# Performance work log

Measured on AMD Instinct MI355X. Metric: run time of the kernel, lower is better.

The kernel has to match this reference:

```python
import jax, jax.numpy as jnp
import numpy as np

B = 32768        # batch
COORD = 64       # entorhinal coordinate dim
DG = 2048        # dentate gyrus dim
CA3 = 256        # CA3 dim
CA1 = 256        # CA1 dim
K_ACTIVE = max(1, int(DG * 0.04))   # = 81, DG top-k sparsity
SETTLE_STEPS = 5
GAIN = 0.7
SIGMA = 2.0      # ca3_distance_sigma
N_EPISODES = 64  # ca3_max_episodes
EC_TAU = 0.5
LN_EPS = 1e-5
COS_EPS = 1e-8


def _build_w_recurrent():
    """Hebbian outer-product weights gated by anatomical distance mask (numpy, deterministic)."""
    rng = np.random.default_rng(0)
    theta = np.linspace(0.0, np.pi, CA3)
    pos = np.stack([3.0 * np.cos(theta),
                    4.0 + np.sin(theta),
                    rng.standard_normal(CA3) * 0.8], axis=-1)
    pos = pos + rng.standard_normal(pos.shape) * 0.15
    diff = pos[None, :, :] - pos[:, None, :]
    dist = np.sqrt((diff ** 2).sum(-1) + 1e-8)
    mask = np.exp(-dist / SIGMA)                       # [CA3, CA3] distance gate
    P = rng.standard_normal((N_EPISODES, CA3)).astype(np.float32)
    P = P / (np.linalg.norm(P, axis=1, keepdims=True) + 1e-8)
    W = P.T @ P                                        # Hebbian pattern storage
    np.fill_diagonal(W, 0.0)
    W = W * mask
    return jnp.asarray(W, dtype=jnp.float32)


def setup_inputs() -> dict:
    key = jax.random.key(0)
    ks = jax.random.split(key, 16)
    def lin(k, out_d, in_d):
        s = 1.0 / np.sqrt(in_d)
        return jax.random.uniform(k, (out_d, in_d), jnp.float32, -s, s)
    return {
        "coords":   jax.random.normal(ks[0], (B, COORD), jnp.float32),
        # EC layernorm
        "ec_gamma": jnp.ones((COORD,), jnp.float32),
        "ec_beta":  jnp.zeros((COORD,), jnp.float32),
        # DG perforant path + layernorm
        "W_pp":     lin(ks[1], DG, COORD),
        "b_pp":     jnp.zeros((DG,), jnp.float32),
        "dg_gamma": jnp.ones((DG,), jnp.float32),
        "dg_beta":  jnp.zeros((DG,), jnp.float32),
        # CA3
        "W_mossy":  lin(ks[2], CA3, DG),
        "W_rec":    _build_w_recurrent(),
        "W_sc":     lin(ks[3], CA1, CA3),
        "b_sc":     jnp.zeros((CA1,), jnp.float32),
        # CA1 comparator
        "W_ta":     lin(ks[4], CA1, COORD),
        "b_ta":     jnp.zeros((CA1,), jnp.float32),
        "W_cs":     lin(ks[5], CA1, CA1),
        "W_cd":     lin(ks[6], CA1, CA1),
        "W_og":     lin(ks[7], CA1, CA1),
        "b_og":     jnp.zeros((CA1,), jnp.float32),
    }


def _layernorm(x, gamma, beta):
    mu = jnp.mean(x, axis=-1, keepdims=True)
    var = jnp.mean(jnp.square(x - mu), axis=-1, keepdims=True)
    return (x - mu) * jax.lax.rsqrt(var + LN_EPS) * gamma + beta


def reference(coords, ec_gamma, ec_beta, W_pp, b_pp, dg_gamma, dg_beta,
              W_mossy, W_rec, W_sc, b_sc, W_ta, b_ta, W_cs, W_cd, W_og, b_og):
    # --- EntorhinalCortex: short-term buffer (no-grad EMA from zero init) + layernorm ---
    buf = EC_TAU * 0.0 + (1.0 - EC_TAU) * jax.lax.stop_gradient(jnp.mean(coords, axis=0))
    ec = _layernorm(coords + 0.1 * buf[None, :], ec_gamma, ec_beta)          # [B, COORD]

    # --- DentateGyrus: relu -> layernorm -> top-k sparsification (scatter) ---
    proj = _layernorm(jax.nn.relu(ec @ W_pp.T + b_pp), dg_gamma, dg_beta)    # [B, DG]
    vals, idx = jax.lax.top_k(proj, K_ACTIVE)                                # [B, K]
    rows = jnp.arange(proj.shape[0])[:, None]
    dg = jnp.zeros_like(proj).at[rows, idx].set(vals)                        # sparse code

    # --- CA3AttractorNetwork: mossy cue + recurrent attractor settle ---
    cue = dg @ W_mossy.T                                                     # [B, CA3]
    state = cue
    for _ in range(SETTLE_STEPS):
        state = jnp.tanh(GAIN * (state @ W_rec.T) + (1.0 - GAIN) * cue)
    ca1_input = state @ W_sc.T + b_sc                                        # [B, CA1]

    # --- CA1Comparator: novelty-gated mix of direct EC path and schaffer input ---
    direct = ec @ W_ta.T + b_ta                                              # [B, CA1]
    s_proj = ca1_input @ W_cs.T
    d_proj = direct @ W_cd.T
    s_n = jnp.maximum(jnp.linalg.norm(s_proj, axis=-1), COS_EPS)
    d_n = jnp.maximum(jnp.linalg.norm(d_proj, axis=-1), COS_EPS)
    cos_sim = jnp.sum(s_proj * d_proj, axis=-1) / (s_n * d_n)
    novelty = jnp.clip(1.0 - cos_sim, 0.0, 1.0)                              # [B]
    gate = novelty[:, None]
    combined = gate * direct + (1.0 - gate) * ca1_input
    ca1_output = jnp.tanh(combined @ W_og.T + b_og)                          # [B, CA1]
    return ca1_output, novelty
```

## Files before the change

### kernel.cpp

```cpp
#include <hip/hip_runtime.h>
#include <hip/hip_bf16.h>
#include <math.h>

#define B_N 32768
#define COORD 64
#define DG 2048
#define CA 256
#define K_ACT 81
#define SETTLE_STEPS 5
#define GAIN 0.7f
#define LN_EPS 1e-5f
#define COS_EPS 1e-8f

__device__ __forceinline__ float wave_sum(float v) {
#pragma unroll
  for (int d = 1; d < 64; d <<= 1) v += __shfl_xor(v, d);
  return v;
}

__device__ __forceinline__ float dot4(float4 a, float4 b) {
  return a.x * b.x + a.y * b.y + a.z * b.z + a.w * b.w;
}

__device__ __forceinline__ void fma4(float4& a, float s, float4 w) {
  a.x += s * w.x; a.y += s * w.y; a.z += s * w.z; a.w += s * w.w;
}

__device__ __forceinline__ unsigned int okey(float f) {
  unsigned int u = __float_as_uint(f);
  return (u & 0x80000000u) ? ~u : (u | 0x80000000u);
}

__global__ void colsum_kernel(const float* __restrict__ coords,
                              float* __restrict__ colsum) {
  int tid = threadIdx.x;
  int col = tid & 63;
  int rg = tid >> 6;
  float s = 0.f;
  int base = blockIdx.x * 128;
#pragma unroll 4
  for (int i = 0; i < 32; ++i) {
    int r = base + rg + i * 4;
    s += coords[r * COORD + col];
  }
  __shared__ float sh[256];
  sh[tid] = s;
  __syncthreads();
  if (tid < 64) {
    float t = sh[tid] + sh[tid + 64] + sh[tid + 128] + sh[tid + 192];
    atomicAdd(&colsum[tid], t);
  }
}

__global__ void transpose_any(const float* __restrict__ S,
                              float* __restrict__ T, int R, int C) {
  int idx = blockIdx.x * 256 + threadIdx.x;
  if (idx < R * C) {
    int r = idx / C, c = idx - r * C;
    T[c * R + r] = S[r * C + c];
  }
}

__global__ __launch_bounds__(512, 4) void mega1(
    const float* __restrict__ coords, const float* __restrict__ colsum,
    const float* __restrict__ ec_gamma, const float* __restrict__ ec_beta,
    const float* __restrict__ W_ppT, const float* __restrict__ b_pp,
    const float* __restrict__ dg_gamma, const float* __restrict__ dg_beta,
    const float* __restrict__ WmT, float* __restrict__ cue_g) {
  __shared__ __align__(16) float proj_s[8][DG];
  __shared__ __align__(16) float ec_s[8][COORD];
  __shared__ unsigned int hist[8][256];
  __shared__ float psum_s[8][8], psq_s[8][8];
  __shared__ int sel_s[8][88];

  const int w = threadIdx.x >> 6;
  const int l = threadIdx.x & 63;
  const int row0 = blockIdx.x * 8;

  {
    int row = row0 + w;
    float x = coords[row * COORD + l] + (0.05f / (float)B_N) * colsum[l];
    float mu = wave_sum(x) * (1.f / 64.f);
    float d = x - mu;
    float var = wave_sum(d * d) * (1.f / 64.f);
    ec_s[w][l] = d * rsqrtf(var + LN_EPS) * ec_gamma[l] + ec_beta[l];
  }
  __syncthreads();

  {
    float4 acc[8];
#pragma unroll
    for (int r = 0; r < 8; ++r) acc[r] = make_float4(0.f, 0.f, 0.f, 0.f);
    const float4* wp4 = reinterpret_cast<const float4*>(W_ppT);
    const int cbase = 64 * w + l;
    for (int kg = 0; kg < 16; ++kg) {
      float4 w40 = wp4[(4 * kg + 0) * 512 + cbase];
      float4 w41 = wp4[(4 * kg + 1) * 512 + cbase];
      float4 w42 = wp4[(4 * kg + 2) * 512 + cbase];
      float4 w43 = wp4[(4 * kg + 3) * 512 + cbase];
#pragma unroll
      for (int r = 0; r < 8; ++r) {
        float4 e4 = reinterpret_cast<const float4*>(ec_s[r])[kg];
        fma4(acc[r], e4.x, w40);
        fma4(acc[r], e4.y, w41);
        fma4(acc[r], e4.z, w42);
        fma4(acc[r], e4.w, w43);
      }
    }
    float4 bp = reinterpret_cast<const float4*>(b_pp)[cbase];
#pragma unroll
    for (int r = 0; r < 8; ++r) {
      float4 h;
      h.x = fmaxf(acc[r].x + bp.x, 0.f);
      h.y = fmaxf(acc[r].y + bp.y, 0.f);
      h.z = fmaxf(acc[r].z + bp.z, 0.f);
      h.w = fmaxf(acc[r].w + bp.w, 0.f);
      reinterpret_cast<float4*>(proj_s[r])[cbase] = h;
      float ps = wave_sum(h.x + h.y + h.z + h.w);
      float pq = wave_sum(dot4(h, h));
      if (l == 0) { psum_s[w][r] = ps; psq_s[w][r] = pq; }
    }
  }
  __syncthreads();

  float mu2, rs2;
  {
    float s = 0.f, q = 0.f;
#pragma unroll
    for (int w2 = 0; w2 < 8; ++w2) { s += psum_s[w2][w]; q += psq_s[w2][w]; }
    mu2 = s * (1.f / (float)DG);
    float var = q * (1.f / (float)DG) - mu2 * mu2;
    rs2 = rsqrtf(var + LN_EPS);
  }
  unsigned int key[32];
#pragma unroll 4
  for (int i = 0; i < 32; ++i) {
    int j = i * 64 + l;
    float v = (proj_s[w][j] - mu2) * rs2 * dg_gamma[j] + dg_beta[j];
    proj_s[w][j] = v;
    key[i] = okey(v);
  }

  unsigned int prefix = 0, rem = K_ACT;
#pragma unroll 1
  for (int pass = 0; pass < 4; ++pass) {
    int sh = 24 - 8 * pass;
#pragma unroll
    for (int b = l; b < 256; b += 64) hist[w][b] = 0;
#pragma unroll 4
    for (int i = 0; i < 32; ++i) {
      unsigned int k = key[i];
      bool ok = (pass == 0) || ((k >> (sh + 8)) == prefix);
      if (ok) atomicAdd(&hist[w][(k >> sh) & 255u], 1u);
    }
    unsigned int h0 = hist[w][4 * l + 0], h1 = hist[w][4 * l + 1];
    unsigned int h2 = hist[w][4 * l + 2], h3 = hist[w][4 * l + 3];
    unsigned int own = h0 + h1 + h2 + h3;
    unsigned int inc = own;
#pragma unroll
    for (int d = 1; d < 64; d <<= 1) {
      unsigned int v = __shfl_down(inc, d);
      if (l + d < 64) inc += v;
    }
    unsigned int cnt = inc - own;
    unsigned int pk = 0;
    {
      unsigned int hb;
      hb = h3; if (cnt < rem && rem <= cnt + hb) pk = ((rem - cnt) << 8) | (unsigned)(4 * l + 3); cnt += hb;
      hb = h2; if (cnt < rem && rem <= cnt + hb) pk = ((rem - cnt) << 8) | (unsigned)(4 * l + 2); cnt += hb;
      hb = h1; if (cnt < rem && rem <= cnt + hb) pk = ((rem - cnt) << 8) | (unsigned)(4 * l + 1); cnt += hb;
      hb = h0; if (cnt < rem && rem <= cnt + hb) pk = ((rem - cnt) << 8) | (unsigned)(4 * l + 0); cnt += hb;
    }
#pragma unroll
    for (int d = 1; d < 64; d <<= 1) pk |= __shfl_xor(pk, d);
    prefix = (prefix << 8) | (pk & 255u);
    rem = pk >> 8;
  }
  const unsigned int Tkey = prefix;
  const unsigned int rem_final = rem;

  const unsigned long long below = (1ull << l) - 1ull;
  int basec = 0;
  unsigned int eq_seen = 0;
  for (int i = 0; i < 32; ++i) {
    int j = i * 64 + l;
    unsigned int k = key[i];
    bool gt = k > Tkey;
    bool eq = (k == Tkey);
    unsigned long long em = __ballot(eq);
    unsigned int eq_before = eq_seen + (unsigned)__popcll(em & below);
    bool sel = gt || (eq && (eq_before < rem_final));
    unsigned long long sm = __ballot(sel);
    int pos = basec + (int)__popcll(sm & below);
    if (sel) sel_s[w][pos] = j;
    basec += (int)__popcll(sm);
    eq_seen += (unsigned)__popcll(em);
  }

  float4 c4 = make_float4(0.f, 0.f, 0.f, 0.f);
  const float4* wm4 = reinterpret_cast<const float4*>(WmT);
  for (int k = 0; k < K_ACT; ++k) {
    int j = sel_s[w][k];
    float v = proj_s[w][j];
    fma4(c4, v, wm4[j * 64 + l]);
  }
  reinterpret_cast<float4*>(cue_g)[(size_t)(row0 + w) * 64 + l] = c4;
}

__global__ __launch_bounds__(256, 2) void mega2(
    const float* __restrict__ coords, const float* __restrict__ colsum,
    const float* __restrict__ ec_gamma, const float* __restrict__ ec_beta,
    const float* __restrict__ cue_g,
    const float* __restrict__ W_recT,
    const float* __restrict__ W_scT, const float* __restrict__ b_sc,
    const float* __restrict__ W_taT, const float* __restrict__ b_ta,
    const float* __restrict__ W_csT, const float* __restrict__ W_cdT,
    const float* __restrict__ W_ogT, const float* __restrict__ b_og,
    float* __restrict__ out) {
  __shared__ __align__(16) float bufA[32][CA];
  __shared__ __align__(16) float bufB[32][CA];
  __shared__ __align__(16) float ec_s[32][COORD];

  const int w = threadIdx.x >> 6;
  const int l = threadIdx.x & 63;
  const int row0 = blockIdx.x * 32 + w * 8;

#pragma unroll 1
  for (int r = 0; r < 8; ++r) {
    int row = row0 + r;
    float x = coords[row * COORD + l] + (0.05f / (float)B_N) * colsum[l];
    float mu = wave_sum(x) * (1.f / 64.f);
    float d = x - mu;
    float var = wave_sum(d * d) * (1.f / 64.f);
    ec_s[w * 8 + r][l] = d * rsqrtf(var + LN_EPS) * ec_gamma[l] + ec_beta[l];
  }

  float4 cu[8];
#pragma unroll
  for (int r = 0; r < 8; ++r) {
    cu[r] = reinterpret_cast<const float4*>(cue_g)[(size_t)(row0 + r) * 64 + l];
    reinterpret_cast<float4*>(bufA[w * 8 + r])[l] = cu[r];
  }

  const float4* wr4 = reinterpret_cast<const float4*>(W_recT);
  float4 acc[8];

#pragma unroll 1
  for (int it = 0; it < SETTLE_STEPS; ++it) {
#pragma unroll
    for (int r = 0; r < 8; ++r) acc[r] = make_float4(0.f, 0.f, 0.f, 0.f);
#pragma unroll 2
    for (int jg = 0; jg < 64; ++jg) {
      float4 w40 = wr4[(4 * jg + 0) * 64 + l];
      float4 w41 = wr4[(4 * jg + 1) * 64 + l];
      float4 w42 = wr4[(4 * jg + 2) * 64 + l];
      float4 w43 = wr4[(4 * jg + 3) * 64 + l];
#pragma unroll
      for (int r = 0; r < 8; ++r) {
        float4 s4 = reinterpret_cast<const float4*>(bufA[w * 8 + r])[jg];
        fma4(acc[r], s4.x, w40);
        fma4(acc[r], s4.y, w41);
        fma4(acc[r], s4.z, w42);
        fma4(acc[r], s4.w, w43);
      }
    }
#pragma unroll
    for (int r = 0; r < 8; ++r) {
      float4 ns;
      ns.x = tanhf(GAIN * acc[r].x + (1.f - GAIN) * cu[r].x);
      ns.y = tanhf(GAIN * acc[r].y + (1.f - GAIN) * cu[r].y);
      ns.z = tanhf(GAIN * acc[r].z + (1.f - GAIN) * cu[r].z);
      ns.w = tanhf(GAIN * acc[r].w + (1.f - GAIN) * cu[r].w);
      reinterpret_cast<float4*>(bufA[w * 8 + r])[l] = ns;
    }
  }

  {
    const float4* ws4 = reinterpret_cast<const float4*>(W_scT);
#pragma unroll
    for (int r = 0; r < 8; ++r) acc[r] = make_float4(0.f, 0.f, 0.f, 0.f);
#pragma unroll 2
    for (int jg = 0; jg < 64; ++jg) {
      float4 w40 = ws4[(4 * jg + 0) * 64 + l];
      float4 w41 = ws4[(4 * jg + 1) * 64 + l];
      float4 w42 = ws4[(4 * jg + 2) * 64 + l];
      float4 w43 = ws4[(4 * jg + 3) * 64 + l];
#pragma unroll
      for (int r = 0; r < 8; ++r) {
        float4 s4 = reinterpret_cast<const float4*>(bufA[w * 8 + r])[jg];
        fma4(acc[r], s4.x, w40);
        fma4(acc[r], s4.y, w41);
        fma4(acc[r], s4.z, w42);
        fma4(acc[r], s4.w, w43);
      }
    }
    float4 bs = reinterpret_cast<const float4*>(b_sc)[l];
#pragma unroll
    for (int r = 0; r < 8; ++r) {
      cu[r].x = acc[r].x + bs.x;
      cu[r].y = acc[r].y + bs.y;
      cu[r].z = acc[r].z + bs.z;
      cu[r].w = acc[r].w + bs.w;
      reinterpret_cast<float4*>(bufB[w * 8 + r])[l] = cu[r];
    }
  }

  float4 dr[8];
  {
    const float4* wt4 = reinterpret_cast<const float4*>(W_taT);
#pragma unroll
    for (int r = 0; r < 8; ++r) acc[r] = make_float4(0.f, 0.f, 0.f, 0.f);
#pragma unroll 2
    for (int kg = 0; kg < 16; ++kg) {
      float4 w40 = wt4[(4 * kg + 0) * 64 + l];
      float4 w41 = wt4[(4 * kg + 1) * 64 + l];
      float4 w42 = wt4[(4 * kg + 2) * 64 + l];
      float4 w43 = wt4[(4 * kg + 3) * 64 + l];
#pragma unroll
      for (int r = 0; r < 8; ++r) {
        float4 e4 = reinterpret_cast<const float4*>(ec_s[w * 8 + r])[kg];
        fma4(acc[r], e4.x, w40);
        fma4(acc[r], e4.y, w41);
        fma4(acc[r], e4.z, w42);
        fma4(acc[r], e4.w, w43);
      }
    }
    float4 bt = reinterpret_cast<const float4*>(b_ta)[l];
#pragma unroll
    for (int r = 0; r < 8; ++r) {
      dr[r].x = acc[r].x + bt.x;
      dr[r].y = acc[r].y + bt.y;
      dr[r].z = acc[r].z + bt.z;
      dr[r].w = acc[r].w + bt.w;
      reinterpret_cast<float4*>(bufA[w * 8 + r])[l] = dr[r];
    }
  }

  float4 dpr[8];
  {
    const float4* wc4 = reinterpret_cast<const float4*>(W_cdT);
#pragma unroll
    for (int r = 0; r < 8; ++r) acc[r] = make_float4(0.f, 0.f, 0.f, 0.f);
#pragma unroll 2
    for (int jg = 0; jg < 64; ++jg) {
      float4 w40 = wc4[(4 * jg + 0) * 64 + l];
      float4 w41 = wc4[(4 * jg + 1) * 64 + l];
      float4 w42 = wc4[(4 * jg + 2) * 64 + l];
      float4 w43 = wc4[(4 * jg + 3) * 64 + l];
#pragma unroll
      for (int r = 0; r < 8; ++r) {
        float4 s4 = reinterpret_cast<const float4*>(bufA[w * 8 + r])[jg];
        fma4(acc[r], s4.x, w40);
        fma4(acc[r], s4.y, w41);
        fma4(acc[r], s4.z, w42);
        fma4(acc[r], s4.w, w43);
      }
    }
#pragma unroll
    for (int r = 0; r < 8; ++r) dpr[r] = acc[r];
  }

  {
    const float4* wc4 = reinterpret_cast<const float4*>(W_csT);
#pragma unroll
    for (int r = 0; r < 8; ++r) acc[r] = make_float4(0.f, 0.f, 0.f, 0.f);
#pragma unroll 2
    for (int jg = 0; jg < 64; ++jg) {
      float4 w40 = wc4[(4 * jg + 0) * 64 + l];
      float4 w41 = wc4[(4 * jg + 1) * 64 + l];
      float4 w42 = wc4[(4 * jg + 2) * 64 + l];
      float4 w43 = wc4[(4 * jg + 3) * 64 + l];
#pragma unroll
      for (int r = 0; r < 8; ++r) {
        float4 s4 = reinterpret_cast<const float4*>(bufB[w * 8 + r])[jg];
        fma4(acc[r], s4.x, w40);
        fma4(acc[r], s4.y, w41);
        fma4(acc[r], s4.z, w42);
        fma4(acc[r], s4.w, w43);
      }
    }
  }

#pragma unroll 1
  for (int r = 0; r < 8; ++r) {
    float sd = wave_sum(dot4(acc[r], dpr[r]));
    float sn = wave_sum(dot4(acc[r], acc[r]));
    float dn = wave_sum(dot4(dpr[r], dpr[r]));
    float s_n = fmaxf(sqrtf(sn), COS_EPS);
    float d_n = fmaxf(sqrtf(dn), COS_EPS);
    float nov = fminf(fmaxf(1.f - sd / (s_n * d_n), 0.f), 1.f);
    float4 cb;
    cb.x = nov * dr[r].x + (1.f - nov) * cu[r].x;
    cb.y = nov * dr[r].y + (1.f - nov) * cu[r].y;
    cb.z = nov * dr[r].z + (1.f - nov) * cu[r].z;
    cb.w = nov * dr[r].w + (1.f - nov) * cu[r].w;
    reinterpret_cast<float4*>(bufA[w * 8 + r])[l] = cb;
    if (l == 0) out[(size_t)B_N * CA + (row0 + r)] = nov;
  }

  {
    const float4* wo4 = reinterpret_cast<const float4*>(W_ogT);
#pragma unroll
    for (int r = 0; r < 8; ++r) acc[r] = make_float4(0.f, 0.f, 0.f, 0.f);
#pragma unroll 2
    for (int jg = 0; jg < 64; ++jg) {
      float4 w40 = wo4[(4 * jg + 0) * 64 + l];
      float4 w41 = wo4[(4 * jg + 1) * 64 + l];
      float4 w42 = wo4[(4 * jg + 2) * 64 + l];
      float4 w43 = wo4[(4 * jg + 3) * 64 + l];
#pragma unroll
      for (int r = 0; r < 8; ++r) {
        float4 s4 = reinterpret_cast<const float4*>(bufA[w * 8 + r])[jg];
        fma4(acc[r], s4.x, w40);
        fma4(acc[r], s4.y, w41);
        fma4(acc[r], s4.z, w42);
        fma4(acc[r], s4.w, w43);
      }
    }
    float4 bo = reinterpret_cast<const float4*>(b_og)[l];
#pragma unroll
    for (int r = 0; r < 8; ++r) {
      float4 o;
      o.x = tanhf(acc[r].x + bo.x);
      o.y = tanhf(acc[r].y + bo.y);
      o.z = tanhf(acc[r].z + bo.z);
      o.w = tanhf(acc[r].w + bo.w);
      reinterpret_cast<float4*>(out)[(size_t)(row0 + r) * 64 + l] = o;
    }
  }
}

extern "C" void kernel_launch(void* const* d_in, const int* in_sizes, int n_in,
                              void* d_out, int out_size, void* d_ws,
                              size_t ws_size, hipStream_t stream) {
  const float* coords = (const float*)d_in[0];
  const float* ec_gamma = (const float*)d_in[1];
  const float* ec_beta = (const float*)d_in[2];
  const float* W_pp = (const float*)d_in[3];
  const float* b_pp = (const float*)d_in[4];
  const float* dg_gamma = (const float*)d_in[5];
  const float* dg_beta = (const float*)d_in[6];
  const float* W_mossy = (const float*)d_in[7];
  const float* W_rec = (const float*)d_in[8];
  const float* W_sc = (const float*)d_in[9];
  const float* b_sc = (const float*)d_in[10];
  const float* W_ta = (const float*)d_in[11];
  const float* b_ta = (const float*)d_in[12];
  const float* W_cs = (const float*)d_in[13];
  const float* W_cd = (const float*)d_in[14];
  const float* W_og = (const float*)d_in[15];
  const float* b_og = (const float*)d_in[16];
  float* out = (float*)d_out;

  float* ws = (float*)d_ws;
  float* colsum = ws;
  float* WmT = colsum + 64;
  float* W_ppT = WmT + 2048 * 256;
  float* W_recT = W_ppT + 64 * 2048;
  float* W_scT = W_recT + 256 * 256;
  float* W_csT = W_scT + 256 * 256;
  float* W_cdT = W_csT + 256 * 256;
  float* W_ogT = W_cdT + 256 * 256;
  float* W_taT = W_ogT + 256 * 256;
  float* cue_g = W_taT + 64 * 256;

  hipMemsetAsync(colsum, 0, COORD * sizeof(float), stream);
  colsum_kernel<<<256, 256, 0, stream>>>(coords, colsum);
  transpose_any<<<(256 * 2048 + 255) / 256, 256, 0, stream>>>(W_mossy, WmT, 256, 2048);
  transpose_any<<<(2048 * 64 + 255) / 256, 256, 0, stream>>>(W_pp, W_ppT, 2048, 64);
  transpose_any<<<(256 * 256 + 255) / 256, 256, 0, stream>>>(W_rec, W_recT, 256, 256);
  transpose_any<<<(256 * 256 + 255) / 256, 256, 0, stream>>>(W_sc, W_scT, 256, 256);
  transpose_any<<<(256 * 256 + 255) / 256, 256, 0, stream>>>(W_cs, W_csT, 256, 256);
  transpose_any<<<(256 * 256 + 255) / 256, 256, 0, stream>>>(W_cd, W_cdT, 256, 256);
  transpose_any<<<(256 * 256 + 255) / 256, 256, 0, stream>>>(W_og, W_ogT, 256, 256);
  transpose_any<<<(256 * 64 + 255) / 256, 256, 0, stream>>>(W_ta, W_taT, 256, 64);

  mega1<<<B_N / 8, 512, 0, stream>>>(coords, colsum, ec_gamma, ec_beta, W_ppT,
                                     b_pp, dg_gamma, dg_beta, WmT, cue_g);
  mega2<<<B_N / 32, 256, 0, stream>>>(coords, colsum, ec_gamma, ec_beta, cue_g,
                                      W_recT, W_scT, b_sc, W_taT, b_ta, W_csT,
                                      W_cdT, W_ogT, b_og, out);
}
```

Measured before the change: 1.059 ms.

## Pre-multiply chained linear weights and replace tanhf with exp-based tanh

Folds the linear chains W_cs·W_sc, W_cd·W_ta, W_og·W_sc and W_og·W_ta into combined weight matrices and bias vectors in small per-call setup kernels. The novelty-gated combine then becomes a linear mix of two precomputed projections, which removes one 256x256 matmul per row and the second shared buffer. tanhf is replaced by an __expf-based formula, and launch bounds are raised to allow more resident blocks. In exchange, floating-point reassociation shifts rounding, and the exp-based tanh can lose accuracy near zero.

```diff
diff --git a/kernel.cpp b/kernel.cpp
--- a/kernel.cpp
+++ b/kernel.cpp
@@ -24,6 +24,11 @@
 
 __device__ __forceinline__ void fma4(float4& a, float s, float4 w) {
   a.x += s * w.x; a.y += s * w.y; a.z += s * w.z; a.w += s * w.w;
+}
+
+__device__ __forceinline__ float fast_tanh(float x) {
+  float e = __expf(2.0f * x);
+  return 1.0f - 2.0f / (e + 1.0f);
 }
 
 __device__ __forceinline__ unsigned int okey(float f) {
@@ -58,6 +63,26 @@
   if (idx < R * C) {
     int r = idx / C, c = idx - r * C;
     T[c * R + r] = S[r * C + c];
+  }
+}
+
+__global__ void fuse_mm(const float* __restrict__ A, const float* __restrict__ BT,
+                        const float* __restrict__ bvec, float* __restrict__ FT,
+                        float* __restrict__ cvec) {
+  __shared__ float brow[256];
+  int in = blockIdx.x, out = threadIdx.x;
+  brow[out] = BT[in * 256 + out];
+  __syncthreads();
+  const float* arow = A + out * 256;
+  float acc = 0.f;
+#pragma unroll 4
+  for (int k = 0; k < 256; ++k) acc += arow[k] * brow[k];
+  FT[in * 256 + out] = acc;
+  if (in == 0) {
+    float b = 0.f;
+#pragma unroll 4
+    for (int k = 0; k < 256; ++k) b += arow[k] * bvec[k];
+    cvec[out] = b;
   }
 }
 
@@ -207,18 +232,16 @@
   reinterpret_cast<float4*>(cue_g)[(size_t)(row0 + w) * 64 + l] = c4;
 }
 
-__global__ __launch_bounds__(256, 2) void mega2(
+__global__ __launch_bounds__(256, 4) void mega2(
     const float* __restrict__ coords, const float* __restrict__ colsum,
     const float* __restrict__ ec_gamma, const float* __restrict__ ec_beta,
-    const float* __restrict__ cue_g,
-    const float* __restrict__ W_recT,
-    const float* __restrict__ W_scT, const float* __restrict__ b_sc,
-    const float* __restrict__ W_taT, const float* __restrict__ b_ta,
-    const float* __restrict__ W_csT, const float* __restrict__ W_cdT,
-    const float* __restrict__ W_ogT, const float* __restrict__ b_og,
-    float* __restrict__ out) {
-  __shared__ __align__(16) float bufA[32][CA];
-  __shared__ __align__(16) float bufB[32][CA];
+    const float* __restrict__ cue_g, const float* __restrict__ W_recT,
+    const float* __restrict__ F1T, const float* __restrict__ c1,
+    const float* __restrict__ F2T, const float* __restrict__ c2,
+    const float* __restrict__ F3T, const float* __restrict__ c3,
+    const float* __restrict__ F4T, const float* __restrict__ c4v,
+    const float* __restrict__ b_og, float* __restrict__ out) {
+  __shared__ __align__(16) float st_s[32][CA];
   __shared__ __align__(16) float ec_s[32][COORD];
 
   const int w = threadIdx.x >> 6;
@@ -239,148 +262,98 @@
 #pragma unroll
   for (int r = 0; r < 8; ++r) {
     cu[r] = reinterpret_cast<const float4*>(cue_g)[(size_t)(row0 + r) * 64 + l];
-    reinterpret_cast<float4*>(bufA[w * 8 + r])[l] = cu[r];
-  }
-
-  const float4* wr4 = reinterpret_cast<const float4*>(W_recT);
+    reinterpret_cast<float4*>(st_s[w * 8 + r])[l] = cu[r];
+  }
+
   float4 acc[8];
 
+  {
+    const float4* wr4 = reinterpret_cast<const float4*>(W_recT);
 #pragma unroll 1
-  for (int it = 0; it < SETTLE_STEPS; ++it) {
+    for (int it = 0; it < SETTLE_STEPS; ++it) {
+#pragma unroll
+      for (int r = 0; r < 8; ++r) acc[r] = make_float4(0.f, 0.f, 0.f, 0.f);
+#pragma unroll 2
+      for (int jg = 0; jg < 64; ++jg) {
+        float4 w40 = wr4[(4 * jg + 0) * 64 + l];
+        float4 w41 = wr4[(4 * jg + 1) * 64 + l];
+        float4 w42 = wr4[(4 * jg + 2) * 64 + l];
+        float4 w43 = wr4[(4 * jg + 3) * 64 + l];
+#pragma unroll
+        for (int r = 0; r < 8; ++r) {
+          float4 s4 = reinterpret_cast<const float4*>(st_s[w * 8 + r])[jg];
+          fma4(acc[r], s4.x, w40);
+          fma4(acc[r], s4.y, w41);
+          fma4(acc[r], s4.z, w42);
+          fma4(acc[r], s4.w, w43);
+        }
+      }
+#pragma unroll
+      for (int r = 0; r < 8; ++r) {
+        float4 ns;
+        ns.x = fast_tanh(GAIN * acc[r].x + (1.f - GAIN) * cu[r].x);
+        ns.y = fast_tanh(GAIN * acc[r].y + (1.f - GAIN) * cu[r].y);
+        ns.z = fast_tanh(GAIN * acc[r].z + (1.f - GAIN) * cu[r].z);
+        ns.w = fast_tanh(GAIN * acc[r].w + (1.f - GAIN) * cu[r].w);
+        reinterpret_cast<float4*>(st_s[w * 8 + r])[l] = ns;
+      }
+    }
+  }
+
+  float4 dpr[8];
+  {
+    const float4* f4 = reinterpret_cast<const float4*>(F2T);
+#pragma unroll
+    for (int r = 0; r < 8; ++r) dpr[r] = make_float4(0.f, 0.f, 0.f, 0.f);
+#pragma unroll 2
+    for (int kg = 0; kg < 16; ++kg) {
+      float4 w40 = f4[(4 * kg + 0) * 64 + l];
+      float4 w41 = f4[(4 * kg + 1) * 64 + l];
+      float4 w42 = f4[(4 * kg + 2) * 64 + l];
+      float4 w43 = f4[(4 * kg + 3) * 64 + l];
+#pragma unroll
+      for (int r = 0; r < 8; ++r) {
+        float4 e4 = reinterpret_cast<const float4*>(ec_s[w * 8 + r])[kg];
+        fma4(dpr[r], e4.x, w40);
+        fma4(dpr[r], e4.y, w41);
+        fma4(dpr[r], e4.z, w42);
+        fma4(dpr[r], e4.w, w43);
+      }
+    }
+    float4 cb = reinterpret_cast<const float4*>(c2)[l];
+#pragma unroll
+    for (int r = 0; r < 8; ++r) {
+      dpr[r].x += cb.x; dpr[r].y += cb.y; dpr[r].z += cb.z; dpr[r].w += cb.w;
+    }
+  }
+
+  {
+    const float4* f4 = reinterpret_cast<const float4*>(F1T);
 #pragma unroll
     for (int r = 0; r < 8; ++r) acc[r] = make_float4(0.f, 0.f, 0.f, 0.f);
 #pragma unroll 2
     for (int jg = 0; jg < 64; ++jg) {
-      float4 w40 = wr4[(4 * jg + 0) * 64 + l];
-      float4 w41 = wr4[(4 * jg + 1) * 64 + l];
-      float4 w42 = wr4[(4 * jg + 2) * 64 + l];
-      float4 w43 = wr4[(4 * jg + 3) * 64 + l];
-#pragma unroll
-      for (int r = 0; r < 8; ++r) {
-        float4 s4 = reinterpret_cast<const float4*>(bufA[w * 8 + r])[jg];
+      float4 w40 = f4[(4 * jg + 0) * 64 + l];
+      float4 w41 = f4[(4 * jg + 1) * 64 + l];
+      float4 w42 = f4[(4 * jg + 2) * 64 + l];
+      float4 w43 = f4[(4 * jg + 3) * 64 + l];
+#pragma unroll
+      for (int r = 0; r < 8; ++r) {
+        float4 s4 = reinterpret_cast<const float4*>(st_s[w * 8 + r])[jg];
         fma4(acc[r], s4.x, w40);
         fma4(acc[r], s4.y, w41);
         fma4(acc[r], s4.z, w42);
         fma4(acc[r], s4.w, w43);
       }
     }
+    float4 cb = reinterpret_cast<const float4*>(c1)[l];
 #pragma unroll
     for (int r = 0; r < 8; ++r) {
-      float4 ns;
-      ns.x = tanhf(GAIN * acc[r].x + (1.f - GAIN) * cu[r].x);
-      ns.y = tanhf(GAIN * acc[r].y + (1.f - GAIN) * cu[r].y);
-      ns.z = tanhf(GAIN * acc[r].z + (1.f - GAIN) * cu[r].z);
-      ns.w = tanhf(GAIN * acc[r].w + (1.f - GAIN) * cu[r].w);
-      reinterpret_cast<float4*>(bufA[w * 8 + r])[l] = ns;
-    }
-  }
-
-  {
-    const float4* ws4 = reinterpret_cast<const float4*>(W_scT);
-#pragma unroll
-    for (int r = 0; r < 8; ++r) acc[r] = make_float4(0.f, 0.f, 0.f, 0.f);
-#pragma unroll 2
-    for (int jg = 0; jg < 64; ++jg) {
-      float4 w40 = ws4[(4 * jg + 0) * 64 + l];
-      float4 w41 = ws4[(4 * jg + 1) * 64 + l];
-      float4 w42 = ws4[(4 * jg + 2) * 64 + l];
-      float4 w43 = ws4[(4 * jg + 3) * 64 + l];
-#pragma unroll
-      for (int r = 0; r < 8; ++r) {
-        float4 s4 = reinterpret_cast<const float4*>(bufA[w * 8 + r])[jg];
-        fma4(acc[r], s4.x, w40);
-        fma4(acc[r], s4.y, w41);
-        fma4(acc[r], s4.z, w42);
-        fma4(acc[r], s4.w, w43);
-      }
-    }
-    float4 bs = reinterpret_cast<const float4*>(b_sc)[l];
-#pragma unroll
-    for (int r = 0; r < 8; ++r) {
-      cu[r].x = acc[r].x + bs.x;
-      cu[r].y = acc[r].y + bs.y;
-      cu[r].z = acc[r].z + bs.z;
-      cu[r].w = acc[r].w + bs.w;
-      reinterpret_cast<float4*>(bufB[w * 8 + r])[l] = cu[r];
-    }
-  }
-
-  float4 dr[8];
-  {
-    const float4* wt4 = reinterpret_cast<const float4*>(W_taT);
-#pragma unroll
-    for (int r = 0; r < 8; ++r) acc[r] = make_float4(0.f, 0.f, 0.f, 0.f);
-#pragma unroll 2
-    for (int kg = 0; kg < 16; ++kg) {
-      float4 w40 = wt4[(4 * kg + 0) * 64 + l];
-      float4 w41 = wt4[(4 * kg + 1) * 64 + l];
-      float4 w42 = wt4[(4 * kg + 2) * 64 + l];
-      float4 w43 = wt4[(4 * kg + 3) * 64 + l];
-#pragma unroll
-      for (int r = 0; r < 8; ++r) {
-        float4 e4 = reinterpret_cast<const float4*>(ec_s[w * 8 + r])[kg];
-        fma4(acc[r], e4.x, w40);
-        fma4(acc[r], e4.y, w41);
-        fma4(acc[r], e4.z, w42);
-        fma4(acc[r], e4.w, w43);
-      }
-    }
-    float4 bt = reinterpret_cast<const float4*>(b_ta)[l];
-#pragma unroll
-    for (int r = 0; r < 8; ++r) {
-      dr[r].x = acc[r].x + bt.x;
-      dr[r].y = acc[r].y + bt.y;
-      dr[r].z = acc[r].z + bt.z;
-      dr[r].w = acc[r].w + bt.w;
-      reinterpret_cast<float4*>(bufA[w * 8 + r])[l] = dr[r];
-    }
-  }
-
-  float4 dpr[8];
-  {
-    const float4* wc4 = reinterpret_cast<const float4*>(W_cdT);
-#pragma unroll
-    for (int r = 0; r < 8; ++r) acc[r] = make_float4(0.f, 0.f, 0.f, 0.f);
-#pragma unroll 2
-    for (int jg = 0; jg < 64; ++jg) {
-      float4 w40 = wc4[(4 * jg + 0) * 64 + l];
-      float4 w41 = wc4[(4 * jg + 1) * 64 + l];
-      float4 w42 = wc4[(4 * jg + 2) * 64 + l];
-      float4 w43 = wc4[(4 * jg + 3) * 64 + l];
-#pragma unroll
-      for (int r = 0; r < 8; ++r) {
-        float4 s4 = reinterpret_cast<const float4*>(bufA[w * 8 + r])[jg];
-        fma4(acc[r], s4.x, w40);
-        fma4(acc[r], s4.y, w41);
-        fma4(acc[r], s4.z, w42);
-        fma4(acc[r], s4.w, w43);
-      }
-    }
-#pragma unroll
-    for (int r = 0; r < 8; ++r) dpr[r] = acc[r];
-  }
-
-  {
-    const float4* wc4 = reinterpret_cast<const float4*>(W_csT);
-#pragma unroll
-    for (int r = 0; r < 8; ++r) acc[r] = make_float4(0.f, 0.f, 0.f, 0.f);
-#pragma unroll 2
-    for (int jg = 0; jg < 64; ++jg) {
-      float4 w40 = wc4[(4 * jg + 0) * 64 + l];
-      float4 w41 = wc4[(4 * jg + 1) * 64 + l];
-      float4 w42 = wc4[(4 * jg + 2) * 64 + l];
-      float4 w43 = wc4[(4 * jg + 3) * 64 + l];
-#pragma unroll
-      for (int r = 0; r < 8; ++r) {
-        float4 s4 = reinterpret_cast<const float4*>(bufB[w * 8 + r])[jg];
-        fma4(acc[r], s4.x, w40);
-        fma4(acc[r], s4.y, w41);
-        fma4(acc[r], s4.z, w42);
-        fma4(acc[r], s4.w, w43);
-      }
-    }
-  }
-
+      acc[r].x += cb.x; acc[r].y += cb.y; acc[r].z += cb.z; acc[r].w += cb.w;
+    }
+  }
+
+  float nov[8];
 #pragma unroll 1
   for (int r = 0; r < 8; ++r) {
     float sd = wave_sum(dot4(acc[r], dpr[r]));
@@ -388,43 +361,65 @@
     float dn = wave_sum(dot4(dpr[r], dpr[r]));
     float s_n = fmaxf(sqrtf(sn), COS_EPS);
     float d_n = fmaxf(sqrtf(dn), COS_EPS);
-    float nov = fminf(fmaxf(1.f - sd / (s_n * d_n), 0.f), 1.f);
-    float4 cb;
-    cb.x = nov * dr[r].x + (1.f - nov) * cu[r].x;
-    cb.y = nov * dr[r].y + (1.f - nov) * cu[r].y;
-    cb.z = nov * dr[r].z + (1.f - nov) * cu[r].z;
-    cb.w = nov * dr[r].w + (1.f - nov) * cu[r].w;
-    reinterpret_cast<float4*>(bufA[w * 8 + r])[l] = cb;
-    if (l == 0) out[(size_t)B_N * CA + (row0 + r)] = nov;
-  }
-
-  {
-    const float4* wo4 = reinterpret_cast<const float4*>(W_ogT);
+    nov[r] = fminf(fmaxf(1.f - sd / (s_n * d_n), 0.f), 1.f);
+    if (l == 0) out[(size_t)B_N * CA + (row0 + r)] = nov[r];
+  }
+
+  {
+    const float4* f4 = reinterpret_cast<const float4*>(F4T);
+#pragma unroll
+    for (int r = 0; r < 8; ++r) dpr[r] = make_float4(0.f, 0.f, 0.f, 0.f);
+#pragma unroll 2
+    for (int kg = 0; kg < 16; ++kg) {
+      float4 w40 = f4[(4 * kg + 0) * 64 + l];
+      float4 w41 = f4[(4 * kg + 1) * 64 + l];
+      float4 w42 = f4[(4 * kg + 2) * 64 + l];
+      float4 w43 = f4[(4 * kg + 3) * 64 + l];
+#pragma unroll
+      for (int r = 0; r < 8; ++r) {
+        float4 e4 = reinterpret_cast<const float4*>(ec_s[w * 8 + r])[kg];
+        fma4(dpr[r], e4.x, w40);
+        fma4(dpr[r], e4.y, w41);
+        fma4(dpr[r], e4.z, w42);
+        fma4(dpr[r], e4.w, w43);
+      }
+    }
+    float4 cb = reinterpret_cast<const float4*>(c4v)[l];
+#pragma unroll
+    for (int r = 0; r < 8; ++r) {
+      dpr[r].x += cb.x; dpr[r].y += cb.y; dpr[r].z += cb.z; dpr[r].w += cb.w;
+    }
+  }
+
+  {
+    const float4* f4 = reinterpret_cast<const float4*>(F3T);
 #pragma unroll
     for (int r = 0; r < 8; ++r) acc[r] = make_float4(0.f, 0.f, 0.f, 0.f);
 #pragma unroll 2
     for (int jg = 0; jg < 64; ++jg) {
-      float4 w40 = wo4[(4 * jg + 0) * 64 + l];
-      float4 w41 = wo4[(4 * jg + 1) * 64 + l];
-      float4 w42 = wo4[(4 * jg + 2) * 64 + l];
-      float4 w43 = wo4[(4 * jg + 3) * 64 + l];
-#pragma unroll
-      for (int r = 0; r < 8; ++r) {
-        float4 s4 = reinterpret_cast<const float4*>(bufA[w * 8 + r])[jg];
+      float4 w40 = f4[(4 * jg + 0) * 64 + l];
+      float4 w41 = f4[(4 * jg + 1) * 64 + l];
+      float4 w42 = f4[(4 * jg + 2) * 64 + l];
+      float4 w43 = f4[(4 * jg + 3) * 64 + l];
+#pragma unroll
+      for (int r = 0; r < 8; ++r) {
+        float4 s4 = reinterpret_cast<const float4*>(st_s[w * 8 + r])[jg];
         fma4(acc[r], s4.x, w40);
         fma4(acc[r], s4.y, w41);
         fma4(acc[r], s4.z, w42);
         fma4(acc[r], s4.w, w43);
       }
     }
+    float4 cc = reinterpret_cast<const float4*>(c3)[l];
     float4 bo = reinterpret_cast<const float4*>(b_og)[l];
 #pragma unroll
     for (int r = 0; r < 8; ++r) {
+      float g = nov[r], h = 1.f - nov[r];
       float4 o;
-      o.x = tanhf(acc[r].x + bo.x);
-      o.y = tanhf(acc[r].y + bo.y);
-      o.z = tanhf(acc[r].z + bo.z);
-      o.w = tanhf(acc[r].w + bo.w);
+      o.x = fast_tanh(g * dpr[r].x + h * (acc[r].x + cc.x) + bo.x);
+      o.y = fast_tanh(g * dpr[r].y + h * (acc[r].y + cc.y) + bo.y);
+      o.z = fast_tanh(g * dpr[r].z + h * (acc[r].z + cc.z) + bo.z);
+      o.w = fast_tanh(g * dpr[r].w + h * (acc[r].w + cc.w) + bo.w);
       reinterpret_cast<float4*>(out)[(size_t)(row0 + r) * 64 + l] = o;
     }
   }
@@ -454,15 +449,20 @@
 
   float* ws = (float*)d_ws;
   float* colsum = ws;
-  float* WmT = colsum + 64;
-  float* W_ppT = WmT + 2048 * 256;
+  float* WmT    = colsum + 64;
+  float* W_ppT  = WmT + 2048 * 256;
   float* W_recT = W_ppT + 64 * 2048;
-  float* W_scT = W_recT + 256 * 256;
-  float* W_csT = W_scT + 256 * 256;
-  float* W_cdT = W_csT + 256 * 256;
-  float* W_ogT = W_cdT + 256 * 256;
-  float* W_taT = W_ogT + 256 * 256;
-  float* cue_g = W_taT + 64 * 256;
+  float* W_scT  = W_recT + 256 * 256;
+  float* W_taT  = W_scT + 256 * 256;
+  float* F1T    = W_taT + 64 * 256;
+  float* F2T    = F1T + 256 * 256;
+  float* F3T    = F2T + 64 * 256;
+  float* F4T    = F3T + 256 * 256;
+  float* c1     = F4T + 64 * 256;
+  float* c2     = c1 + 256;
+  float* c3     = c2 + 256;
+  float* c4     = c3 + 256;
+  float* cue_g  = c4 + 256;
 
   hipMemsetAsync(colsum, 0, COORD * sizeof(float), stream);
   colsum_kernel<<<256, 256, 0, stream>>>(coords, colsum);
@@ -470,14 +470,16 @@
   transpose_any<<<(2048 * 64 + 255) / 256, 256, 0, stream>>>(W_pp, W_ppT, 2048, 64);
   transpose_any<<<(256 * 256 + 255) / 256, 256, 0, stream>>>(W_rec, W_recT, 256, 256);
   transpose_any<<<(256 * 256 + 255) / 256, 256, 0, stream>>>(W_sc, W_scT, 256, 256);
-  transpose_any<<<(256 * 256 + 255) / 256, 256, 0, stream>>>(W_cs, W_csT, 256, 256);
-  transpose_any<<<(256 * 256 + 255) / 256, 256, 0, stream>>>(W_cd, W_cdT, 256, 256);
-  transpose_any<<<(256 * 256 + 255) / 256, 256, 0, stream>>>(W_og, W_ogT, 256, 256);
   transpose_any<<<(256 * 64 + 255) / 256, 256, 0, stream>>>(W_ta, W_taT, 256, 64);
+
+  fuse_mm<<<256, 256, 0, stream>>>(W_cs, W_scT, b_sc, F1T, c1);
+  fuse_mm<<<64, 256, 0, stream>>>(W_cd, W_taT, b_ta, F2T, c2);
+  fuse_mm<<<256, 256, 0, stream>>>(W_og, W_scT, b_sc, F3T, c3);
+  fuse_mm<<<64, 256, 0, stream>>>(W_og, W_taT, b_ta, F4T, c4);
 
   mega1<<<B_N / 8, 512, 0, stream>>>(coords, colsum, ec_gamma, ec_beta, W_ppT,
                                      b_pp, dg_gamma, dg_beta, WmT, cue_g);
   mega2<<<B_N / 32, 256, 0, stream>>>(coords, colsum, ec_gamma, ec_beta, cue_g,
-                                      W_recT, W_scT, b_sc, W_taT, b_ta, W_csT,
-                                      W_cdT, W_ogT, b_og, out);
-}
+                                      W_recT, F1T, c1, F2T, c2, F3T, c3, F4T,
+                                      c4, b_og, out);
+}
```

Measured after the change: 1.099 ms. +3.8%, slower.
